# Optimization experiments

Hardware: AMD Instinct MI355X
Metric: run time of the kernel (lower is better)

## Reference

```python
import jax, jax.numpy as jnp
import numpy as np

D, B, V = 8, 4096, 1024          # token fields (type..section), batch streams, vocab per field
THRES = 0.9                      # top_k filter_thres default
TEMP = 1.0                       # temperature default
NOTE_TYPE = 1                    # note_type_code; sos=0, eos=2


def setup_inputs() -> dict:
    key = jax.random.key(0)
    k1, k2, k3 = jax.random.split(key, 3)
    logits = jax.random.normal(k1, (D, B, V), dtype=jnp.float32)
    u = jax.random.uniform(k2, (D, B, V), dtype=jnp.float32)
    current_values = jax.random.randint(k3, (D, B), 0, 16).astype(jnp.int32)
    return {"logits": logits, "u": u, "current_values": current_values}


def reference(logits, u, current_values):
    neg = -jnp.inf
    ar = jnp.arange(V)
    # monotonicity mask: positions < current value are forbidden  [D,B,V]
    lg = jnp.where(ar[None, None, :] < current_values[:, :, None], neg, logits)
    # index 0 is masked for every field (logits[d][:, 0] = -inf in the loop)
    lg = lg.at[:, :, 0].set(neg)
    # top-k filtering: keep values >= k-th largest, k = int((1 - thres) * V)
    k = int((1.0 - THRES) * V)
    kth = jax.lax.top_k(lg, k)[0][..., -1:]          # [D,B,1]
    filt = jnp.where(lg < kth, neg, lg)
    logp = jax.nn.log_softmax(filt / TEMP, axis=-1)  # stable softmax, -inf -> prob 0
    probs = jnp.exp(logp)
    # multinomial sampling via Gumbel-max using provided uniform noise
    eps = 1e-20
    gumbel = -jnp.log(-jnp.log(u + eps) + eps)
    samples = jnp.argmax(logp + gumbel, axis=-1)     # [D,B]
    # type-conditional fill: fields 1..7 are zero unless sampled type == NOTE
    is_note = samples[0] == NOTE_TYPE                # [B]
    keep = (jnp.arange(D)[:, None] == 0) | is_note[None, :]
    tokens = jnp.where(keep, samples, 0)             # [D,B]
    return tokens.T, probs                           # [B,D] int, [D,B,V] float
```

## Files before the change

### kernel.cpp

```cpp
#include <hip/hip_runtime.h>
#include <math.h>

#define DD 8
#define BB 4096
#define VV 1024
#define K_SEL 102
#define RPB 4

__device__ __forceinline__ unsigned f2key(float f) {
    unsigned u = __float_as_uint(f);
    unsigned m = (unsigned)((int)u >> 31) | 0x80000000u;
    return u ^ m;
}
__device__ __forceinline__ float key2f(unsigned k) {
    unsigned m = 0x80000000u | ~((unsigned)((int)k >> 31));
    return __uint_as_float(k ^ m);
}

__global__ __launch_bounds__(256) void decode_row_kernel(
    const float* __restrict__ logits,
    const float* __restrict__ unoise,
    const int* __restrict__ curvals,
    float* __restrict__ probs_out,
    int* __restrict__ samples)
{
    const int wave = threadIdx.x >> 6;
    const int lane = threadIdx.x & 63;
    const int row  = blockIdx.x * RPB + wave;

    __shared__ __align__(16) unsigned hist[RPB][1040];
    unsigned* h = hist[wave];

    const float4* l4 = (const float4*)(logits + (size_t)row * VV);
    const float4* u4 = (const float4*)(unoise + (size_t)row * VV);
    const int cv = curvals[row];

    unsigned key[16];
#pragma unroll
    for (int i = 0; i < 4; i++) {
        float4 f = l4[i * 64 + lane];
        const int vb = i * 256 + lane * 4;
        float e[4] = {f.x, f.y, f.z, f.w};
#pragma unroll
        for (int j = 0; j < 4; j++) {
            int v = vb + j;
            float t = (v < cv || v == 0) ? -INFINITY : e[j];
            key[i * 4 + j] = f2key(t);
        }
    }

    unsigned prefix = 0;
    unsigned kk = K_SEL;
    const int rep = (lane & 3) * 260;
#pragma unroll
    for (int pass = 0; pass < 4; pass++) {
        const int shift = 24 - 8 * pass;
        const uint4 z = {0u, 0u, 0u, 0u};
#pragma unroll
        for (int r = 0; r < 4; r++)
            ((uint4*)(h + r * 260))[lane] = z;
        __builtin_amdgcn_wave_barrier();
#pragma unroll
        for (int i = 0; i < 16; i++) {
            bool act = (pass == 0) ||
                       (((key[i] ^ prefix) >> ((shift + 8) & 31)) == 0);
            if (act) atomicAdd(h + rep + ((key[i] >> shift) & 0xFFu), 1u);
        }
        __threadfence_block();
        __builtin_amdgcn_wave_barrier();
        uint4 c0 = ((uint4*)(h + 0 * 260))[lane];
        uint4 c1 = ((uint4*)(h + 1 * 260))[lane];
        uint4 c2 = ((uint4*)(h + 2 * 260))[lane];
        uint4 c3 = ((uint4*)(h + 3 * 260))[lane];
        __builtin_amdgcn_wave_barrier();
        unsigned cnt0 = c0.x + c1.x + c2.x + c3.x;
        unsigned cnt1 = c0.y + c1.y + c2.y + c3.y;
        unsigned cnt2 = c0.z + c1.z + c2.z + c3.z;
        unsigned cnt3 = c0.w + c1.w + c2.w + c3.w;
        unsigned s3 = cnt3;
        unsigned s2 = cnt2 + s3;
        unsigned s1 = cnt1 + s2;
        unsigned s0 = cnt0 + s1;
        unsigned suf = s0;
#pragma unroll
        for (int off = 1; off < 64; off <<= 1) {
            unsigned o = __shfl_down(suf, off, 64);
            suf += (lane + off < 64) ? o : 0u;
        }
        const unsigned above = suf - s0;
        unsigned sel = 0u;
        bool found = false;
        {
            unsigned ge, gt;
            ge = s0 + above; gt = ge - cnt0;
            if (ge >= kk && gt < kk) { found = true; sel = ((unsigned)(lane * 4 + 0) << 16) | (kk - gt); }
            ge = s1 + above; gt = ge - cnt1;
            if (ge >= kk && gt < kk) { found = true; sel = ((unsigned)(lane * 4 + 1) << 16) | (kk - gt); }
            ge = s2 + above; gt = ge - cnt2;
            if (ge >= kk && gt < kk) { found = true; sel = ((unsigned)(lane * 4 + 2) << 16) | (kk - gt); }
            ge = s3 + above; gt = ge - cnt3;
            if (ge >= kk && gt < kk) { found = true; sel = ((unsigned)(lane * 4 + 3) << 16) | (kk - gt); }
        }
        unsigned long long bal = __ballot(found);
        int src = __ffsll((unsigned long long)bal) - 1;
        sel = __shfl(sel, src, 64);
        prefix |= (sel >> 16) << shift;
        kk = sel & 0xFFFFu;
        __builtin_amdgcn_wave_barrier();
    }

    unsigned mk = key[0];
#pragma unroll
    for (int i = 1; i < 16; i++) mk = max(mk, key[i]);
#pragma unroll
    for (int off = 32; off; off >>= 1)
        mk = max(mk, (unsigned)__shfl_xor(mk, off, 64));
    const float m = key2f(mk);

    float ex[16];
    float s = 0.0f;
#pragma unroll
    for (int i = 0; i < 16; i++) {
        bool keep = key[i] >= prefix;
        float e = keep ? __expf(key2f(key[i]) - m) : 0.0f;
        ex[i] = e;
        s += e;
    }
#pragma unroll
    for (int off = 32; off; off >>= 1)
        s += __shfl_xor(s, off, 64);

    const float lz  = __logf(s);
    const float inv = 1.0f / s;
    const float mlz = m + lz;

    float bestv = -INFINITY;
    int   besti = VV;
    float4* p4 = (float4*)(probs_out + (size_t)row * VV);
#pragma unroll
    for (int i = 0; i < 4; i++) {
        float4 uu = u4[i * 64 + lane];
        float4 pv;
        pv.x = ex[i * 4 + 0] * inv;
        pv.y = ex[i * 4 + 1] * inv;
        pv.z = ex[i * 4 + 2] * inv;
        pv.w = ex[i * 4 + 3] * inv;
        p4[i * 64 + lane] = pv;
        float us[4] = {uu.x, uu.y, uu.z, uu.w};
#pragma unroll
        for (int j = 0; j < 4; j++) {
            const int idx = i * 4 + j;
            bool keep = key[idx] >= prefix;
            float lp = keep ? (key2f(key[idx]) - mlz) : -INFINITY;
            float g = -__logf(-__logf(us[j] + 1e-20f) + 1e-20f);
            float sc = lp + g;
            int v = i * 256 + lane * 4 + j;
            if (sc > bestv) { bestv = sc; besti = v; }
        }
    }
#pragma unroll
    for (int off = 32; off; off >>= 1) {
        float ov = __shfl_xor(bestv, off, 64);
        int   oi = __shfl_xor(besti, off, 64);
        if (ov > bestv || (ov == bestv && oi < besti)) { bestv = ov; besti = oi; }
    }
    if (lane == 0) samples[row] = besti;
}

__global__ __launch_bounds__(256) void tokens_kernel(
    const int* __restrict__ samples, float* __restrict__ tokens_out)
{
    int i = blockIdx.x * 256 + threadIdx.x;
    int b = i >> 3;
    int d = i & 7;
    int sm = samples[d * BB + b];
    int t0 = samples[b];
    tokens_out[i] = (d == 0 || t0 == 1) ? (float)sm : 0.0f;
}

extern "C" void kernel_launch(void* const* d_in, const int* in_sizes, int n_in,
                              void* d_out, int out_size, void* d_ws, size_t ws_size,
                              hipStream_t stream) {
    const float* logits = (const float*)d_in[0];
    const float* unoise = (const float*)d_in[1];
    const int*   curvals = (const int*)d_in[2];

    float* out        = (float*)d_out;
    float* tokens_out = out;
    float* probs_out  = out + (size_t)BB * DD;
    int*   samples    = (int*)d_ws;

    decode_row_kernel<<<(DD * BB) / RPB, 256, 0, stream>>>(logits, unoise, curvals,
                                                           probs_out, samples);
    tokens_kernel<<<(BB * DD) / 256, 256, 0, stream>>>(samples, tokens_out);
}
```

Measured before the change: 319.5 us.

## Cut radix select to two passes and sample via ratio comparison without logs

Reduces the 8-bit radix select for the top-k threshold from four histogram passes to two. It then resolves the remaining candidates sharing the top 16 bits with an iterative wave-wide max/count loop. Sampling replaces the Gumbel-max log-of-log score with an equivalent comparison of exp(x-m)/(-log u) via cross-multiplication, which drops one log per element and the log of the sum. Noise loads are also hoisted ahead of the reduction. The risks are a data-dependent loop for tied or clustered candidates and slight rounding differences from the ratio comparison.

```diff
diff --git a/kernel.cpp b/kernel.cpp
--- a/kernel.cpp
+++ b/kernel.cpp
@@ -33,18 +33,20 @@
 
     const float4* l4 = (const float4*)(logits + (size_t)row * VV);
     const float4* u4 = (const float4*)(unoise + (size_t)row * VV);
-    const int cv = curvals[row];
+    const int cv1 = max(curvals[row], 1);
 
     unsigned key[16];
+    float    fv[16];
 #pragma unroll
     for (int i = 0; i < 4; i++) {
-        float4 f = l4[i * 64 + lane];
+        float4 ff = l4[i * 64 + lane];
         const int vb = i * 256 + lane * 4;
-        float e[4] = {f.x, f.y, f.z, f.w};
+        float e[4] = {ff.x, ff.y, ff.z, ff.w};
 #pragma unroll
         for (int j = 0; j < 4; j++) {
             int v = vb + j;
-            float t = (v < cv || v == 0) ? -INFINITY : e[j];
+            float t = (v < cv1) ? -INFINITY : e[j];
+            fv[i * 4 + j]  = t;
             key[i * 4 + j] = f2key(t);
         }
     }
@@ -53,7 +55,7 @@
     unsigned kk = K_SEL;
     const int rep = (lane & 3) * 260;
 #pragma unroll
-    for (int pass = 0; pass < 4; pass++) {
+    for (int pass = 0; pass < 2; pass++) {
         const int shift = 24 - 8 * pass;
         const uint4 z = {0u, 0u, 0u, 0u};
 #pragma unroll
@@ -62,9 +64,9 @@
         __builtin_amdgcn_wave_barrier();
 #pragma unroll
         for (int i = 0; i < 16; i++) {
-            bool act = (pass == 0) ||
-                       (((key[i] ^ prefix) >> ((shift + 8) & 31)) == 0);
-            if (act) atomicAdd(h + rep + ((key[i] >> shift) & 0xFFu), 1u);
+            unsigned t = (key[i] ^ prefix) >> shift;
+            unsigned inc = (pass == 0) ? 1u : (t < 256u ? 1u : 0u);
+            atomicAdd(h + rep + (t & 0xFFu), inc);
         }
         __threadfence_block();
         __builtin_amdgcn_wave_barrier();
@@ -109,60 +111,86 @@
         __builtin_amdgcn_wave_barrier();
     }
 
-    unsigned mk = key[0];
-#pragma unroll
-    for (int i = 1; i < 16; i++) mk = max(mk, key[i]);
+    unsigned cmask = 0u;
+#pragma unroll
+    for (int i = 0; i < 16; i++)
+        if ((key[i] & 0xFFFF0000u) == prefix) cmask |= (1u << i);
+    unsigned thr;
+    for (;;) {
+        unsigned mx = 0u;
+#pragma unroll
+        for (int i = 0; i < 16; i++)
+            if (cmask & (1u << i)) mx = max(mx, key[i]);
+#pragma unroll
+        for (int off = 32; off; off >>= 1)
+            mx = max(mx, (unsigned)__shfl_xor((int)mx, off, 64));
+        if (kk <= 1u) { thr = mx; break; }
+        unsigned ceq = 0u;
+#pragma unroll
+        for (int i = 0; i < 16; i++)
+            if (key[i] == mx) ceq++;
+#pragma unroll
+        for (int off = 32; off; off >>= 1)
+            ceq += (unsigned)__shfl_xor((int)ceq, off, 64);
+        if (kk <= ceq) { thr = mx; break; }
+        kk -= ceq;
+#pragma unroll
+        for (int i = 0; i < 16; i++)
+            if (key[i] == mx) cmask &= ~(1u << i);
+    }
+    const float thrf = key2f(thr);
+
+    float m = fv[0];
+#pragma unroll
+    for (int i = 1; i < 16; i++) m = fmaxf(m, fv[i]);
 #pragma unroll
     for (int off = 32; off; off >>= 1)
-        mk = max(mk, (unsigned)__shfl_xor(mk, off, 64));
-    const float m = key2f(mk);
+        m = fmaxf(m, __shfl_xor(m, off, 64));
 
     float ex[16];
     float s = 0.0f;
 #pragma unroll
     for (int i = 0; i < 16; i++) {
-        bool keep = key[i] >= prefix;
-        float e = keep ? __expf(key2f(key[i]) - m) : 0.0f;
+        float e = (fv[i] >= thrf) ? __expf(fv[i] - m) : 0.0f;
         ex[i] = e;
         s += e;
     }
+    float4 uu[4];
+#pragma unroll
+    for (int i = 0; i < 4; i++) uu[i] = u4[i * 64 + lane];
 #pragma unroll
     for (int off = 32; off; off >>= 1)
         s += __shfl_xor(s, off, 64);
-
-    const float lz  = __logf(s);
     const float inv = 1.0f / s;
-    const float mlz = m + lz;
-
-    float bestv = -INFINITY;
+
+    float bnum = 0.0f, bden = 1.0f;
     int   besti = VV;
     float4* p4 = (float4*)(probs_out + (size_t)row * VV);
 #pragma unroll
     for (int i = 0; i < 4; i++) {
-        float4 uu = u4[i * 64 + lane];
         float4 pv;
         pv.x = ex[i * 4 + 0] * inv;
         pv.y = ex[i * 4 + 1] * inv;
         pv.z = ex[i * 4 + 2] * inv;
         pv.w = ex[i * 4 + 3] * inv;
         p4[i * 64 + lane] = pv;
-        float us[4] = {uu.x, uu.y, uu.z, uu.w};
+        float us[4] = {uu[i].x, uu[i].y, uu[i].z, uu[i].w};
 #pragma unroll
         for (int j = 0; j < 4; j++) {
             const int idx = i * 4 + j;
-            bool keep = key[idx] >= prefix;
-            float lp = keep ? (key2f(key[idx]) - mlz) : -INFINITY;
-            float g = -__logf(-__logf(us[j] + 1e-20f) + 1e-20f);
-            float sc = lp + g;
+            float nl = 1e-20f - __logf(us[j] + 1e-20f);
+            float a  = ex[idx];
             int v = i * 256 + lane * 4 + j;
-            if (sc > bestv) { bestv = sc; besti = v; }
+            if (a * bden > bnum * nl) { bnum = a; bden = nl; besti = v; }
         }
     }
 #pragma unroll
     for (int off = 32; off; off >>= 1) {
-        float ov = __shfl_xor(bestv, off, 64);
-        int   oi = __shfl_xor(besti, off, 64);
-        if (ov > bestv || (ov == bestv && oi < besti)) { bestv = ov; besti = oi; }
+        float onum = __shfl_xor(bnum, off, 64);
+        float oden = __shfl_xor(bden, off, 64);
+        int   oi   = __shfl_xor(besti, off, 64);
+        float x = onum * bden, y = bnum * oden;
+        if (x > y || (x == y && oi < besti)) { bnum = onum; bden = oden; besti = oi; }
     }
     if (lane == 0) samples[row] = besti;
 }
```

Result: no change. 317.0 us (-0.8%).
